# Performance work log

Measured on AMD Instinct MI355X. Metric: run time of the kernel, lower is better.

The kernel has to match this reference:

```python
import math
import jax, jax.numpy as jnp
import numpy as np
from jax import lax

B, S, D = 2, 1024, 768
H, E, DH = 12, 8, 64          # n_head, num_experts, head dim
KA = 1                        # top-k experts per head (attention)
KF = 2                        # top-k experts per token (FFN)
DFF = 2048
EMA_DECAY = 0.99
CAP_FACTOR = 1.25
NEG_INF = -1e9


def setup_inputs() -> dict:
    key = jax.random.key(0)
    ks = jax.random.split(key, 16)
    sc = 0.02
    x = jax.random.normal(ks[0], (B, S, D), jnp.float32)
    causal = jnp.tril(jnp.ones((S, S), jnp.float32))
    mask = jnp.where(causal > 0, 0.0, NEG_INF).astype(jnp.float32)
    return {
        "x": x,
        "mask": mask,
        "W_q": jax.random.normal(ks[1], (D, D), jnp.float32) * sc,
        "W_k": jax.random.normal(ks[2], (D, D), jnp.float32) * sc,
        "W_v": jax.random.normal(ks[3], (H, E, DH, DH), jnp.float32) * sc,
        "W_o": jax.random.normal(ks[4], (H, E, DH, DH), jnp.float32) * sc,
        "W_router": jax.random.normal(ks[5], (D, H * E), jnp.float32) * sc,
        "g1": jnp.ones((D,), jnp.float32),
        "b1": jnp.zeros((D,), jnp.float32),
        "g2": jnp.ones((D,), jnp.float32),
        "b2": jnp.zeros((D,), jnp.float32),
        "gate_ff": jax.random.normal(ks[6], (D, E), jnp.float32) * sc,
        "W1": jax.random.normal(ks[7], (E, D, DFF), jnp.float32) * sc,
        "W2": jax.random.normal(ks[8], (E, DFF, D), jnp.float32) * sc,
    }


def layer_norm(x, g, b, eps=1e-5):
    m = jnp.mean(x, -1, keepdims=True)
    v = jnp.var(x, -1, keepdims=True)
    return (x - m) * lax.rsqrt(v + eps) * g + b


def head_switch_attention(x, mask, W_q, W_k, W_v, W_o, W_router):
    b, s, d = x.shape
    q = (x @ W_q).reshape(b, s, H, DH)
    k = (x @ W_k).reshape(b, s, H, DH)
    scores = jnp.einsum("bshd,bthd->bhst", q, k) / math.sqrt(DH) + mask
    p_attn = jax.nn.softmax(scores, axis=-1)          # (B,H,S,S)
    gate_logits = (x @ W_router).reshape(b, s, H, E)
    topk_scores, topk_idx = lax.top_k(gate_logits, KA)  # (B,S,H,KA)
    probs = jax.nn.softmax(topk_scores, axis=-1)
    x_h = x.reshape(b, s, H, DH)
    # value projections for all experts (small d_h x d_h GEMMs)
    v_all = jnp.einsum("bshd,hedf->bshef", x_h, W_v)
    y = jnp.zeros_like(x_h)
    hard_counts = jnp.zeros((H, E), jnp.float32)
    for slot in range(KA):
        oh = jax.nn.one_hot(topk_idx[..., slot], E, dtype=x.dtype)  # (B,S,H,E)
        v_sel = jnp.einsum("bshef,bshe->bshf", v_all, oh)
        # faithful to original einsum 'bhst,hbsd->hbtd' (sums over s)
        attn_out = jnp.einsum("bhst,bshf->bthf", p_attn, v_sel)
        o_all = jnp.einsum("bthf,hefg->btheg", attn_out, W_o)
        o_sel = jnp.einsum("btheg,bthe->bthg", o_all, oh)
        y = y + o_sel * probs[..., slot][..., None]
        hard_counts = hard_counts + lax.stop_gradient(oh).sum((0, 1))
    y = y.reshape(b, s, d)
    # EMA buffers start at zero -> ema = (1-decay)*hard/denom
    ema = hard_counts / (b * s * KA) * (1.0 - EMA_DECAY)
    p_lb = ema / (ema.sum() + 1e-9)
    aux = (p_lb * p_lb).sum() * E * H
    return y, aux


def moe_ffn(x, gate_ff, W1, W2):
    b, s, d = x.shape
    gate_logits = x @ gate_ff                      # (B,S,E), eval: no noise
    topk_scores, topk_idx = lax.top_k(gate_logits, KF)
    probs = jax.nn.softmax(topk_scores, axis=-1)   # (B,S,KF)
    capacity = math.ceil(CAP_FACTOR * (b * s) / E)
    flat_idx = topk_idx.reshape(-1)                # (B*S*KF,)
    oh_flat = jax.nn.one_hot(flat_idx, E, dtype=jnp.float32)
    tokens_so_far = jnp.cumsum(oh_flat, axis=0)
    keep = jnp.take_along_axis(tokens_so_far <= capacity, flat_idx[:, None], axis=1)[:, 0]
    probs = probs * keep.reshape(b, s, KF).astype(probs.dtype)
    probs = probs / (probs.sum(-1, keepdims=True) + 1e-9)
    oh = jax.nn.one_hot(topk_idx, E, dtype=probs.dtype)   # (B,S,KF,E)
    w = (probs[..., None] * oh).sum(2).reshape(b * s, E)  # combined weight per (token, expert)
    xf = x.reshape(b * s, d)
    yf = jnp.zeros_like(xf)
    for e in range(E):
        # scaling applied BEFORE ReLU, matching original x_sel = x * weight
        xe = xf * w[:, e:e + 1]
        yf = yf + jnp.maximum(xe @ W1[e], 0.0) @ W2[e]
    token_ctr = ((probs > 0)[..., None].astype(jnp.float32) * oh).sum((0, 1, 2))
    imp_ctr = (probs[..., None] * oh).sum((0, 1, 2))
    aux = ((token_ctr / token_ctr.sum()) * (imp_ctr / imp_ctr.sum())).sum() * E
    return yf.reshape(b, s, d), aux


def reference(x, mask, W_q, W_k, W_v, W_o, W_router, g1, b1, g2, b2, gate_ff, W1, W2):
    # pre-norm transformer block: x + Attn(LN(x)); x + MoEFFN(LN(x))
    a, aux1 = head_switch_attention(layer_norm(x, g1, b1), mask, W_q, W_k, W_v, W_o, W_router)
    x1 = x + a  # dropout is identity in eval
    f, aux2 = moe_ffn(layer_norm(x1, g2, b2), gate_ff, W1, W2)
    return x1 + f, aux1 + aux2
```

## Files before the change

kernel.cpp:

```cpp
#include <hip/hip_runtime.h>
#include <hip/hip_bf16.h>
#include <cstdint>

typedef __hip_bfloat16 bf16;
typedef __attribute__((ext_vector_type(8))) __bf16 bfrag;
typedef __attribute__((ext_vector_type(4))) float f32x4;

#define B_    2
#define S_    1024
#define D_    768
#define H_    12
#define E_    8
#define DH_   64
#define DFF_  2048
#define CAP_  320
#define CAPP_ 384
#define NTOK  (B_*S_)
#define NTH   (NTOK*H_)
#define QKLD  1536
#define NHE   (H_*E_)

__device__ __forceinline__ void stage16(const bf16* g, bf16* ldsLane){
#if __has_builtin(__builtin_amdgcn_global_load_lds)
  __builtin_amdgcn_global_load_lds((const __attribute__((address_space(1))) unsigned int*)g,
                                   (__attribute__((address_space(3))) unsigned int*)ldsLane, 16, 0, 0);
#else
  *(bfrag*)ldsLane = *(const bfrag*)g;
#endif
}

__global__ __launch_bounds__(256)
void transp_qk(const float* __restrict__ Wq, const float* __restrict__ Wk, bf16* __restrict__ dst)
{
  const float* src = blockIdx.z ? Wk : Wq;
  int rowOff = blockIdx.z ? 768 : 0;
  __shared__ float t[32][33];
  int n0 = blockIdx.x*32, k0 = blockIdx.y*32;
  int tx = threadIdx.x & 31, ty = threadIdx.x >> 5;
#pragma unroll
  for (int r=0;r<4;r++)
    t[ty+r*8][tx] = src[(long)(k0 + ty + r*8)*D_ + n0 + tx];
  __syncthreads();
#pragma unroll
  for (int r=0;r<4;r++)
    dst[(long)(rowOff + n0 + ty + r*8)*D_ + k0 + tx] = __float2bfloat16(t[tx][ty+r*8]);
}

__global__ __launch_bounds__(256)
void transp_cvt(const float* __restrict__ src, bf16* __restrict__ dst,
                int K, int N, long sSrc, long sDst, int dstRowOff)
{
  src += (long)blockIdx.z*sSrc;
  dst += (long)blockIdx.z*sDst;
  __shared__ float t[32][33];
  int n0 = blockIdx.x*32, k0 = blockIdx.y*32;
  int tx = threadIdx.x & 31, ty = threadIdx.x >> 5;
#pragma unroll
  for (int r=0;r<4;r++){
    int kk = k0 + ty + r*8, nn = n0 + tx;
    t[ty+r*8][tx] = (nn < N) ? src[(long)kk*N + nn] : 0.f;
  }
  __syncthreads();
#pragma unroll
  for (int r=0;r<4;r++){
    int nn = n0 + ty + r*8;
    if (nn < N) dst[(long)(dstRowOff + nn)*K + k0 + tx] = __float2bfloat16(t[tx][ty+r*8]);
  }
}

__global__ __launch_bounds__(256)
void transp_f32(const float* __restrict__ src, float* __restrict__ dst, int K, int N)
{
  __shared__ float t[32][33];
  int n0 = blockIdx.x*32, k0 = blockIdx.y*32;
  int tx = threadIdx.x & 31, ty = threadIdx.x >> 5;
#pragma unroll
  for (int r=0;r<4;r++){
    int kk = k0 + ty + r*8, nn = n0 + tx;
    t[ty+r*8][tx] = (nn < N) ? src[(long)kk*N + nn] : 0.f;
  }
  __syncthreads();
#pragma unroll
  for (int r=0;r<4;r++){
    int nn = n0 + ty + r*8;
    if (nn < N) dst[(long)nn*K + k0 + tx] = t[tx][ty+r*8];
  }
}

__global__ __launch_bounds__(256)
void gemm_bn64(const bf16* __restrict__ A, const bf16* __restrict__ Bt,
               void* __restrict__ C, void* __restrict__ C2,
               int M, int N, int K, long sA, long sB, long sC, int relu, int outBf, int kSplit)
{
  int nwg = gridDim.x*gridDim.y*gridDim.z;
  int bid = blockIdx.x + gridDim.x*(blockIdx.y + gridDim.y*blockIdx.z);
  int nid = (bid & 7)*(nwg >> 3) + (bid >> 3);
  int bx = nid % gridDim.x;
  int t1 = nid / gridDim.x;
  int by = t1 % gridDim.y;
  int bz = t1 / gridDim.y;
  int e  = bz / kSplit, kc = bz - e*kSplit;
  A  += (long)e*sA;
  Bt += (long)e*sB;
  int kLen = K / kSplit, kBase = kc*kLen;
  int m0 = by*128, n0 = bx*64;
  __shared__ bf16 As[2][128*32];
  __shared__ bf16 Bs[2][64*32];
  int tid = threadIdx.x;
  int w = tid >> 6, lane = tid & 63;
  int quad = lane >> 4, l16 = lane & 15;
  int wm = w*32;
  f32x4 acc[2][4] = {};
  int srow = (lane >> 2);
  int gsw  = ((lane & 3) ^ (srow & 3))*8;
  const bf16* aBase = A + (long)m0*K;
  const bf16* bBase = Bt + (long)n0*K;
  int xr = (l16 & 3);
  int nIt = kLen >> 5;
  {
    int k0 = kBase;
#pragma unroll
    for (int j=0;j<2;j++){
      int c = w*2 + j, row = c*16 + srow;
      stage16(aBase + (long)row*K + k0 + gsw, As[0] + c*512 + lane*8);
    }
    int rowb = w*16 + srow;
    stage16(bBase + (long)rowb*K + k0 + gsw, Bs[0] + w*512 + lane*8);
  }
  int cur = 0;
  for (int it=0; it<nIt; ++it){
    __syncthreads();
    if (it+1 < nIt){
      int k0 = kBase + (it+1)*32;
      int nb = cur^1;
#pragma unroll
      for (int j=0;j<2;j++){
        int c = w*2 + j, row = c*16 + srow;
        stage16(aBase + (long)row*K + k0 + gsw, As[nb] + c*512 + lane*8);
      }
      int rowb = w*16 + srow;
      stage16(bBase + (long)rowb*K + k0 + gsw, Bs[nb] + w*512 + lane*8);
    }
    const bf16* Ac = As[cur];
    const bf16* Bc = Bs[cur];
    bfrag af[2], bfv[4];
#pragma unroll
    for (int t=0;t<2;t++) af[t]  = *(const bfrag*)(Ac + (wm + t*16 + l16)*32 + ((quad ^ xr)*8));
#pragma unroll
    for (int t=0;t<4;t++) bfv[t] = *(const bfrag*)(Bc + (t*16 + l16)*32 + ((quad ^ xr)*8));
#pragma unroll
    for (int ti=0;ti<2;ti++)
#pragma unroll
      for (int tj=0;tj<4;tj++)
        acc[ti][tj] = __builtin_amdgcn_mfma_f32_16x16x32_bf16(af[ti], bfv[tj], acc[ti][tj], 0, 0, 0);
    cur ^= 1;
  }
  long zoff = (long)e*sC;
  void* Cp = kc ? C2 : C;
  if (outBf){
    bf16* Cb = (bf16*)Cp + zoff;
#pragma unroll
    for (int ti=0;ti<2;ti++)
#pragma unroll
      for (int tj=0;tj<4;tj++)
#pragma unroll
        for (int r=0;r<4;r++){
          int row = m0 + wm + ti*16 + quad*4 + r;
          int col = n0 + tj*16 + l16;
          float v = acc[ti][tj][r];
          if (relu) v = fmaxf(v, 0.f);
          Cb[(long)row*N + col] = __float2bfloat16(v);
        }
  } else {
    float* Cf = (float*)Cp + zoff;
#pragma unroll
    for (int ti=0;ti<2;ti++)
#pragma unroll
      for (int tj=0;tj<4;tj++)
#pragma unroll
        for (int r=0;r<4;r++){
          int row = m0 + wm + ti*16 + quad*4 + r;
          int col = n0 + tj*16 + l16;
          float v = acc[ti][tj][r];
          if (relu) v = fmaxf(v, 0.f);
          Cf[(long)row*N + col] = v;
        }
  }
}

__global__ __launch_bounds__(256)
void ln_kernel(const float* __restrict__ src, const float* __restrict__ g, const float* __restrict__ bb,
               float* __restrict__ dstF, bf16* __restrict__ dstB,
               const float* __restrict__ gateW, float* __restrict__ glog2)
{
  int row = blockIdx.x, tid = threadIdx.x;
  __shared__ float red[256];
  __shared__ float gsum[4][E_];
  float v[3];
#pragma unroll
  for (int j=0;j<3;j++) v[j] = src[(long)row*D_ + tid + j*256];
  float s = v[0]+v[1]+v[2];
  red[tid]=s; __syncthreads();
  for (int o=128;o>0;o>>=1){ if(tid<o) red[tid]+=red[tid+o]; __syncthreads(); }
  float mean = red[0]*(1.0f/D_);
  __syncthreads();
  float sq = 0.f;
#pragma unroll
  for (int j=0;j<3;j++){ float d=v[j]-mean; sq += d*d; }
  red[tid]=sq; __syncthreads();
  for (int o=128;o>0;o>>=1){ if(tid<o) red[tid]+=red[tid+o]; __syncthreads(); }
  float rstd = rsqrtf(red[0]*(1.0f/D_) + 1e-5f);
  float ov[3];
#pragma unroll
  for (int j=0;j<3;j++){
    int d = tid + j*256;
    float o = (v[j]-mean)*rstd*g[d] + bb[d];
    ov[j] = o;
    dstF[(long)row*D_+d] = o;
    if (dstB) dstB[(long)row*D_+d] = __float2bfloat16(o);
  }
  if (gateW){
    float gp[E_] = {};
#pragma unroll
    for (int j=0;j<3;j++){
      int d = tid + j*256;
      const float* gw = gateW + (long)d*E_;
#pragma unroll
      for (int e=0;e<E_;e++) gp[e] += ov[j]*gw[e];
    }
#pragma unroll
    for (int off=1; off<64; off<<=1)
#pragma unroll
      for (int e=0;e<E_;e++) gp[e] += __shfl_xor(gp[e], off);
    if ((tid & 63) == 0)
#pragma unroll
      for (int e=0;e<E_;e++) gsum[tid>>6][e] = gp[e];
    __syncthreads();
    if (tid < E_)
      glog2[(long)row*E_ + tid] = gsum[0][tid]+gsum[1][tid]+gsum[2][tid]+gsum[3][tid];
  }
}

#define RTOK 4
__global__ __launch_bounds__(768)
void router_argmax(const float* __restrict__ ln1, const float* __restrict__ WrT,
                   int* __restrict__ eidx, int* __restrict__ gHist,
                   int* __restrict__ hCnt, int* __restrict__ hList)
{
  int tok0 = blockIdx.x*RTOK;
  int tid = threadIdx.x;
  int col = tid >> 3, seg = tid & 7;
  __shared__ float xrow[RTOK][D_];
  __shared__ float logits[RTOK][96];
  for (int i=tid; i<RTOK*D_; i+=768){
    int t = i / D_, dpos = i - t*D_;
    xrow[t][dpos] = ln1[(long)(tok0+t)*D_ + dpos];
  }
  __syncthreads();
  const float* wrow = WrT + (long)col*D_;
  float acc[RTOK] = {};
#pragma unroll
  for (int j=0;j<24;j++){
    int dbase = j*32 + seg*4;
    float4 w = *(const float4*)(wrow + dbase);
#pragma unroll
    for (int t=0;t<RTOK;t++){
      float4 xv = *(const float4*)(&xrow[t][dbase]);
      acc[t] += xv.x*w.x + xv.y*w.y + xv.z*w.z + xv.w*w.w;
    }
  }
#pragma unroll
  for (int off=1; off<8; off<<=1)
#pragma unroll
    for (int t=0;t<RTOK;t++) acc[t] += __shfl_xor(acc[t], off);
  if (seg == 0)
#pragma unroll
    for (int t=0;t<RTOK;t++) logits[t][col] = acc[t];
  __syncthreads();
  if (tid < RTOK*H_){
    int t = tid / H_, h = tid % H_;
    const float* p = &logits[t][h*8];
    float best = p[0]; int bi = 0;
#pragma unroll
    for (int e=1;e<8;e++){ float v=p[e]; if (v > best){ best=v; bi=e; } }
    int tok = tok0 + t;
    eidx[tok*H_ + h] = bi;
    atomicAdd(&gHist[h*E_ + bi], 1);
    int he = h*E_ + bi;
    int pos = atomicAdd(&hCnt[he], 1);
    hList[he*NTOK + pos] = tok;
  }
}

__global__ __launch_bounds__(256)
void vsel_b(const float* __restrict__ ln1, const float* __restrict__ Wv,
            const int* __restrict__ hCnt, const int* __restrict__ hList,
            bf16* __restrict__ vT)
{
  int he = blockIdx.x;
  int h = he >> 3;
  __shared__ float Ws[DH_*DH_];
  __shared__ float xsh[4][DH_];
  int tid = threadIdx.x;
  const float* W = Wv + (long)he*DH_*DH_;
  for (int i=tid; i<DH_*DH_; i+=256) Ws[i] = W[i];
  int cnt = hCnt[he];
  __syncthreads();
  int w = tid >> 6, lane = tid & 63;
  const int* lst = hList + (long)he*NTOK;
  for (int i = blockIdx.y*4 + w; i < cnt; i += 32){
    int tok = lst[i];
    int b = tok >> 10, s = tok & 1023;
    xsh[w][lane] = ln1[(long)tok*D_ + h*DH_ + lane];
    float acc = 0.f;
#pragma unroll 8
    for (int d=0; d<DH_; d++) acc += xsh[w][d]*Ws[d*DH_ + lane];
    vT[((long)(b*H_+h)*DH_ + lane)*S_ + s] = __float2bfloat16(acc);
  }
}

__global__ __launch_bounds__(256)
void attn_stats_mfma(const bf16* __restrict__ qkB, float* __restrict__ gM, float* __restrict__ gL)
{
  int s0 = blockIdx.x*64;
  int h = blockIdx.y, b = blockIdx.z;
  int tid = threadIdx.x;
  int w = tid >> 6, lane = tid & 63;
  int quad = lane >> 4, l16 = lane & 15;
  int x7 = l16 & 7;
  __shared__ bf16 ldsQ[64*64];
  __shared__ bf16 ldsK[2][64*64];
  const bf16* qbase = qkB + ((long)(b*S_ + s0))*QKLD + h*DH_;
  const bf16* kbase = qkB + ((long)(b*S_))*QKLD + 768 + h*DH_;
#pragma unroll
  for (int j=0;j<2;j++){
    int c = j*256 + tid;
    int row = c >> 3;
    int gs = ((c & 7) ^ (row & 7))*8;
    stage16(qbase + (long)row*QKLD + gs, ldsQ + c*8);
    stage16(kbase + (long)row*QKLD + gs, ldsK[0] + c*8);
  }
  float m_ln[4] = {-1e30f,-1e30f,-1e30f,-1e30f};
  float l_ln[4] = {0.f,0.f,0.f,0.f};
  int ttEnd = s0 >> 6;
  int cur = 0;
  for (int tt=0; tt<=ttEnd; tt++){
    __syncthreads();
    if (tt < ttEnd){
#pragma unroll
      for (int j=0;j<2;j++){
        int c = j*256 + tid;
        int row = c >> 3;
        int gs = ((c & 7) ^ (row & 7))*8;
        stage16(kbase + (long)((tt+1)*64 + row)*QKLD + gs, ldsK[cur^1] + c*8);
      }
    }
    const bf16* Kc = ldsK[cur];
    bfrag af0 = *(const bfrag*)(ldsQ + (w*16 + l16)*64 + ((quad     ^ x7)*8));
    bfrag af1 = *(const bfrag*)(ldsQ + (w*16 + l16)*64 + (((quad+4) ^ x7)*8));
    f32x4 cfr[4];
#pragma unroll
    for (int j=0;j<4;j++){
      bfrag b0 = *(const bfrag*)(Kc + (j*16 + l16)*64 + ((quad     ^ x7)*8));
      bfrag b1 = *(const bfrag*)(Kc + (j*16 + l16)*64 + (((quad+4) ^ x7)*8));
      f32x4 z = {};
      z = __builtin_amdgcn_mfma_f32_16x16x32_bf16(af0, b0, z, 0,0,0);
      z = __builtin_amdgcn_mfma_f32_16x16x32_bf16(af1, b1, z, 0,0,0);
      cfr[j] = z;
    }
#pragma unroll
    for (int r=0;r<4;r++){
      int s_g = s0 + w*16 + quad*4 + r;
      float v0 = (tt*64      + l16 <= s_g) ? cfr[0][r]*0.125f : -1e30f;
      float v1 = (tt*64 + 16 + l16 <= s_g) ? cfr[1][r]*0.125f : -1e30f;
      float v2 = (tt*64 + 32 + l16 <= s_g) ? cfr[2][r]*0.125f : -1e30f;
      float v3 = (tt*64 + 48 + l16 <= s_g) ? cfr[3][r]*0.125f : -1e30f;
      float mt = fmaxf(fmaxf(v0,v1), fmaxf(v2,v3));
      float mn = fmaxf(m_ln[r], mt);
      l_ln[r] = l_ln[r]*__expf(m_ln[r]-mn)
              + ((__expf(v0-mn)+__expf(v1-mn)) + (__expf(v2-mn)+__expf(v3-mn)));
      m_ln[r] = mn;
    }
    cur ^= 1;
  }
  float m_run[4], l_run[4];
#pragma unroll
  for (int r=0;r<4;r++){
    float mf = m_ln[r];
#pragma unroll
    for (int mm=1; mm<16; mm<<=1) mf = fmaxf(mf, __shfl_xor(mf, mm));
    float lf = l_ln[r]*__expf(m_ln[r]-mf);
#pragma unroll
    for (int mm=1; mm<16; mm<<=1) lf += __shfl_xor(lf, mm);
    m_run[r] = mf; l_run[r] = lf;
  }
  if (l16 == 0){
    long base = ((long)(b*H_ + h))*S_ + s0 + w*16 + quad*4;
#pragma unroll
    for (int r=0;r<4;r++){ gM[base+r] = m_run[r]; gL[base+r] = l_run[r]; }
  }
}

__global__ __launch_bounds__(256)
void attn_pv(const bf16* __restrict__ qkB, const bf16* __restrict__ vT,
             const float* __restrict__ gM, const float* __restrict__ gL, float* __restrict__ aoH)
{
  int t0 = blockIdx.x*64;
  int h = blockIdx.y, b = blockIdx.z;
  int bh = b*H_ + h;
  int tid = threadIdx.x;
  int w = tid >> 6, lane = tid & 63;
  int quad = lane >> 4, l16 = lane & 15;
  int x7 = l16 & 7;
  __shared__ bf16 ldsK[64*64];
  __shared__ bf16 ldsQ[2][64*64];
  __shared__ bf16 ldsV[2][64*64];
  __shared__ bf16 ldsS[64*72];
  __shared__ float smx[2][64], sli[2][64];
  const bf16* kbase = qkB + ((long)(b*S_ + t0))*QKLD + 768 + h*DH_;
  const bf16* qbase = qkB + ((long)(b*S_))*QKLD + h*DH_;
  const bf16* vbase = vT + ((long)bh*DH_)*S_;
  int sb0 = t0 >> 6;
#pragma unroll
  for (int j=0;j<2;j++){
    int c = j*256 + tid;
    int row = c >> 3;
    int gs = ((c & 7) ^ (row & 7))*8;
    stage16(kbase + (long)row*QKLD + gs, ldsK + c*8);
    stage16(qbase + (long)(sb0*64 + row)*QKLD + gs, ldsQ[0] + c*8);
    stage16(vbase + (long)row*S_ + sb0*64 + gs, ldsV[0] + c*8);
  }
  if (tid < 64){
    smx[0][tid] = gM[(long)bh*S_ + sb0*64 + tid];
    sli[0][tid] = 1.0f / gL[(long)bh*S_ + sb0*64 + tid];
  }
  f32x4 accO[4] = {};
  int cur = 0;
  for (int sb = sb0; sb < S_/64; sb++){
    __syncthreads();
    if (sb+1 < S_/64){
      int nb = cur^1;
#pragma unroll
      for (int j=0;j<2;j++){
        int c = j*256 + tid;
        int row = c >> 3;
        int gs = ((c & 7) ^ (row & 7))*8;
        stage16(qbase + (long)((sb+1)*64 + row)*QKLD + gs, ldsQ[nb] + c*8);
        stage16(vbase + (long)row*S_ + (sb+1)*64 + gs, ldsV[nb] + c*8);
      }
      if (tid < 64){
        smx[nb][tid] = gM[(long)bh*S_ + (sb+1)*64 + tid];
        sli[nb][tid] = 1.0f / gL[(long)bh*S_ + (sb+1)*64 + tid];
      }
    }
    const bf16* Qc = ldsQ[cur];
    const bf16* Vc = ldsV[cur];
    bfrag af0 = *(const bfrag*)(ldsK + (w*16 + l16)*64 + ((quad     ^ x7)*8));
    bfrag af1 = *(const bfrag*)(ldsK + (w*16 + l16)*64 + (((quad+4) ^ x7)*8));
    f32x4 cs[4];
#pragma unroll
    for (int j=0;j<4;j++){
      bfrag b0 = *(const bfrag*)(Qc + (j*16 + l16)*64 + ((quad     ^ x7)*8));
      bfrag b1 = *(const bfrag*)(Qc + (j*16 + l16)*64 + (((quad+4) ^ x7)*8));
      f32x4 z = {};
      z = __builtin_amdgcn_mfma_f32_16x16x32_bf16(af0, b0, z, 0,0,0);
      z = __builtin_amdgcn_mfma_f32_16x16x32_bf16(af1, b1, z, 0,0,0);
      cs[j] = z;
    }
#pragma unroll
    for (int j=0;j<4;j++)
#pragma unroll
      for (int r=0;r<4;r++){
        int t_loc = w*16 + quad*4 + r;
        int s_loc = j*16 + l16;
        float wgt = ((t0 + t_loc) <= (sb*64 + s_loc))
                  ? __expf(cs[j][r]*0.125f - smx[cur][s_loc])*sli[cur][s_loc] : 0.f;
        ldsS[t_loc*72 + s_loc] = __float2bfloat16(wgt);
      }
    bfrag pa0 = *(const bfrag*)(ldsS + (w*16 + l16)*72 + quad*8);
    bfrag pa1 = *(const bfrag*)(ldsS + (w*16 + l16)*72 + 32 + quad*8);
#pragma unroll
    for (int j=0;j<4;j++){
      bfrag b0 = *(const bfrag*)(Vc + (j*16 + l16)*64 + ((quad     ^ x7)*8));
      bfrag b1 = *(const bfrag*)(Vc + (j*16 + l16)*64 + (((quad+4) ^ x7)*8));
      accO[j] = __builtin_amdgcn_mfma_f32_16x16x32_bf16(pa0, b0, accO[j], 0,0,0);
      accO[j] = __builtin_amdgcn_mfma_f32_16x16x32_bf16(pa1, b1, accO[j], 0,0,0);
    }
    cur ^= 1;
  }
#pragma unroll
  for (int j=0;j<4;j++)
#pragma unroll
    for (int r=0;r<4;r++){
      int t_loc = w*16 + quad*4 + r;
      int f = j*16 + l16;
      aoH[((long)bh*S_ + t0 + t_loc)*DH_ + f] = accO[j][r];
    }
}

__global__ __launch_bounds__(256)
void oproj_b(const float* __restrict__ aoH, const float* __restrict__ Wo,
             const int* __restrict__ hCnt, const int* __restrict__ hList,
             const float* __restrict__ x, float* __restrict__ x1)
{
  int he = blockIdx.x;
  int h = he >> 3;
  __shared__ float Ws[DH_*DH_];
  __shared__ float xsh[4][DH_];
  int tid = threadIdx.x;
  const float* W = Wo + (long)he*DH_*DH_;
  for (int i=tid; i<DH_*DH_; i+=256) Ws[i] = W[i];
  int cnt = hCnt[he];
  __syncthreads();
  int w = tid >> 6, lane = tid & 63;
  const int* lst = hList + (long)he*NTOK;
  for (int i = blockIdx.y*4 + w; i < cnt; i += 32){
    int tok = lst[i];
    int b = tok >> 10, s = tok & 1023;
    xsh[w][lane] = aoH[((long)(b*H_+h)*S_ + s)*DH_ + lane];
    float acc = 0.f;
#pragma unroll 8
    for (int f=0; f<DH_; f++) acc += xsh[w][f]*Ws[f*DH_ + lane];
    long idx = (long)tok*D_ + h*DH_ + lane;
    x1[idx] = x[idx] + acc;
  }
}

__global__ __launch_bounds__(256)
void route_kernel(const float* __restrict__ glog2, const int* __restrict__ gHist,
                  int* __restrict__ gI0, int* __restrict__ gI1,
                  int* __restrict__ gPos0, int* __restrict__ gPos1,
                  int* __restrict__ listTok, float* __restrict__ listW,
                  int* __restrict__ gCnt, float* __restrict__ auxOut)
{
  __shared__ unsigned char sI0[NTOK], sI1[NTOK];
  __shared__ float sP0[NTOK], sP1[NTOK];
  __shared__ short sPos0[NTOK], sPos1[NTOK];
  __shared__ int   sScan[256*E_];
  __shared__ int   sHist[H_*E_];
  __shared__ float sImp[E_];
  __shared__ int   sCnt[E_];
  int tid = threadIdx.x;
  if (tid < E_) sImp[tid] = 0.f;
  if (tid < H_*E_) sHist[tid] = gHist[tid];
  for (int i=tid; i<NTOK; i+=256){
    const float* p = glog2 + (long)i*E_;
    float b0 = p[0]; int e0 = 0;
#pragma unroll
    for (int e=1;e<E_;e++){ float vv=p[e]; if (vv > b0){ b0=vv; e0=e; } }
    float b1v = -1e30f; int e1 = 0;
#pragma unroll
    for (int e=0;e<E_;e++){ if (e==e0) continue; float vv=p[e]; if (vv > b1v){ b1v=vv; e1=e; } }
    float ex = __expf(b1v - b0);
    float inv = 1.f/(1.f + ex);
    sI0[i] = (unsigned char)e0; sI1[i] = (unsigned char)e1;
    sP0[i] = inv; sP1[i] = ex*inv;
    gI0[i] = e0; gI1[i] = e1;
  }
  __syncthreads();
  {
    int myCnt[E_] = {};
#pragma unroll
    for (int j=0;j<16;j++){
      int i = tid*16 + j;
      int tok = i >> 1;
      int e = (i & 1) ? (int)sI1[tok] : (int)sI0[tok];
      myCnt[e]++;
    }
#pragma unroll
    for (int e=0;e<E_;e++) sScan[tid*E_+e] = myCnt[e];
    __syncthreads();
    for (int off=1; off<256; off<<=1){
      int v[E_];
      if (tid >= off){
#pragma unroll
        for (int e=0;e<E_;e++) v[e] = sScan[(tid-off)*E_+e];
      }
      __syncthreads();
      if (tid >= off){
#pragma unroll
        for (int e=0;e<E_;e++) sScan[tid*E_+e] += v[e];
      }
      __syncthreads();
    }
    int pref[E_];
#pragma unroll
    for (int e=0;e<E_;e++) pref[e] = tid ? sScan[(tid-1)*E_+e] : 0;
#pragma unroll
    for (int j=0;j<16;j++){
      int i = tid*16 + j;
      int tok = i >> 1;
      int e = (i & 1) ? (int)sI1[tok] : (int)sI0[tok];
      int pos = pref[e]++;
      short p = (pos < CAP_) ? (short)pos : (short)-1;
      if (i & 1) sPos1[tok] = p; else sPos0[tok] = p;
    }
    if (tid < E_){
      int cnt = sScan[255*E_ + tid];
      sCnt[tid] = cnt < CAP_ ? cnt : CAP_;
      gCnt[tid] = sCnt[tid];
    }
  }
  __syncthreads();
  for (int i=tid; i<NTOK; i+=256){
    int e0 = sI0[i], e1 = sI1[i];
    int p0i = sPos0[i], p1i = sPos1[i];
    float k0 = p0i >= 0 ? 1.f : 0.f, k1 = p1i >= 0 ? 1.f : 0.f;
    float p0 = sP0[i], p1 = sP1[i];
    float denom = p0*k0 + p1*k1 + 1e-9f;
    float w0 = p0*k0/denom, w1 = p1*k1/denom;
    if (p0i >= 0){ listTok[e0*CAP_+p0i] = i; listW[e0*CAP_+p0i] = w0; atomicAdd(&sImp[e0], w0); }
    if (p1i >= 0){ listTok[e1*CAP_+p1i] = i; listW[e1*CAP_+p1i] = w1; atomicAdd(&sImp[e1], w1); }
    gPos0[i] = p0i; gPos1[i] = p1i;
  }
  __syncthreads();
  if (tid == 0){
    float tot = 0.f;
    for (int i=0;i<H_*E_;i++) tot += (float)sHist[i]*(1.0f/NTOK)*0.01f;
    float a1 = 0.f;
    for (int i=0;i<H_*E_;i++){
      float p = ((float)sHist[i]*(1.0f/NTOK)*0.01f)/(tot + 1e-9f);
      a1 += p*p;
    }
    a1 *= (float)(H_*E_);
    float tcs = 0.f, ims = 0.f;
    for (int e=0;e<E_;e++){ tcs += (float)sCnt[e]; ims += sImp[e]; }
    float a2 = 0.f;
    for (int e=0;e<E_;e++) a2 += ((float)sCnt[e]/tcs)*(sImp[e]/ims);
    a2 *= (float)E_;
    auxOut[0] = a1 + a2;
  }
}

__global__ __launch_bounds__(256)
void gather_kernel(const float* __restrict__ ln2, const int* __restrict__ listTok,
                   const float* __restrict__ listW, const int* __restrict__ gCnt,
                   bf16* __restrict__ Xg)
{
  int blk = blockIdx.x;
  int e = blk / CAPP_, r = blk % CAPP_;
  int tid = threadIdx.x;
  bool live = r < gCnt[e];
  int tok = 0; float w = 0.f;
  if (live){ tok = listTok[e*CAP_+r]; w = listW[e*CAP_+r]; }
  for (int d=tid; d<D_; d+=256)
    Xg[(long)blk*D_ + d] = __float2bfloat16(live ? ln2[(long)tok*D_+d]*w : 0.f);
}

__global__ __launch_bounds__(256)
void combine_kernel(const float* __restrict__ x1,
                    const float* __restrict__ Ya, const float* __restrict__ Yb,
                    const int* __restrict__ gI0, const int* __restrict__ gI1,
                    const int* __restrict__ gPos0, const int* __restrict__ gPos1,
                    float* __restrict__ out)
{
  int i = blockIdx.x;
  int tid = threadIdx.x;
  int p0 = gPos0[i], p1 = gPos1[i];
  int e0 = gI0[i],  e1 = gI1[i];
  long off0 = (long)(e0*CAPP_ + (p0 >= 0 ? p0 : 0))*D_;
  long off1 = (long)(e1*CAPP_ + (p1 >= 0 ? p1 : 0))*D_;
  const float* y0a = Ya + off0; const float* y0b = Yb + off0;
  const float* y1a = Ya + off1; const float* y1b = Yb + off1;
  for (int d=tid; d<D_; d+=256){
    float v = x1[(long)i*D_+d];
    if (p0 >= 0) v += y0a[d] + y0b[d];
    if (p1 >= 0) v += y1a[d] + y1b[d];
    out[(long)i*D_+d] = v;
  }
}

extern "C" void kernel_launch(void* const* d_in, const int* in_sizes, int n_in,
                              void* d_out, int out_size, void* d_ws, size_t ws_size,
                              hipStream_t stream)
{
  const float* x    = (const float*)d_in[0];
  const float* W_q  = (const float*)d_in[2];
  const float* W_k  = (const float*)d_in[3];
  const float* W_v  = (const float*)d_in[4];
  const float* W_o  = (const float*)d_in[5];
  const float* W_r  = (const float*)d_in[6];
  const float* g1   = (const float*)d_in[7];
  const float* b1   = (const float*)d_in[8];
  const float* g2   = (const float*)d_in[9];
  const float* b2   = (const float*)d_in[10];
  const float* gate = (const float*)d_in[11];
  const float* W1   = (const float*)d_in[12];
  const float* W2   = (const float*)d_in[13];
  float* out = (float*)d_out;

  float* wsf = (float*)d_ws;
  const long oX1   = 0;
  const long oLnF  = 1572864;
  const long oLnB  = 3145728;
  const long oWcat = 3932160;
  const long oWrT  = 4521984;
  const long oHist = 4595712;
  const long oGM   = 4718592;
  const long oGL   = 4743168;
  const long oEidx = 4767744;
  const long oGlg2 = 4792320;
  const long oI0   = 4808704;
  const long oI1   = 4810752;
  const long oP0   = 4812800;
  const long oP1   = 4814848;
  const long oLT   = 4816896;
  const long oLW   = 4819456;
  const long oCnt  = 4822016;
  const long oHCnt = 4822100;
  const long SB    = 4822528;
  const long TOTAL = SB + 12976128;
  if (ws_size < (size_t)TOTAL*4) return;

  float* x1    = wsf + oX1;
  float* lnbF  = wsf + oLnF;
  bf16*  lnbB  = (bf16*)(wsf + oLnB);
  bf16*  WcatB = (bf16*)(wsf + oWcat);
  float* WrT   = wsf + oWrT;
  int*   gHist = (int*)(wsf + oHist);
  float* gM    = wsf + oGM;
  float* gL    = wsf + oGL;
  int*   eidx  = (int*)(wsf + oEidx);
  float* glog2 = wsf + oGlg2;
  int*   gI0   = (int*)(wsf + oI0);
  int*   gI1   = (int*)(wsf + oI1);
  int*   gPos0 = (int*)(wsf + oP0);
  int*   gPos1 = (int*)(wsf + oP1);
  int*   lTok  = (int*)(wsf + oLT);
  float* lW    = wsf + oLW;
  int*   gCnt  = (int*)(wsf + oCnt);
  int*   hCnt  = (int*)(wsf + oHCnt);
  bf16*  qkB   = (bf16*)(wsf + SB);
  bf16*  vT    = (bf16*)(wsf + SB + 1572864);
  float* aoH   = wsf + SB + 2359296;
  int*   hList = (int*)(wsf + SB + 3932160);
  bf16*  WT    = (bf16*)(wsf + SB);
  bf16*  Xg    = (bf16*)(wsf + SB + 6291456);
  bf16*  Hid   = (bf16*)(wsf + SB + 7471104);
  float* Yexp  = wsf + SB + 10616832;
  float* YexpB = wsf + oLnF;

  hipMemsetAsync(gHist, 0, H_*E_*sizeof(int), stream);
  hipMemsetAsync(hCnt, 0, NHE*sizeof(int), stream);
  transp_qk<<<dim3(24,24,2),256,0,stream>>>(W_q, W_k, WcatB);
  transp_f32<<<dim3(3,24,1),256,0,stream>>>(W_r, WrT, 768, 96);

  ln_kernel<<<NTOK,256,0,stream>>>(x, g1, b1, lnbF, lnbB, nullptr, nullptr);
  gemm_bn64<<<dim3(24,16,1),256,0,stream>>>(lnbB, WcatB, qkB, nullptr, 2048, QKLD, 768, 0,0,0, 0, 1, 1);
  router_argmax<<<NTOK/RTOK,768,0,stream>>>(lnbF, WrT, eidx, gHist, hCnt, hList);
  vsel_b<<<dim3(NHE,8,1),256,0,stream>>>(lnbF, W_v, hCnt, hList, vT);
  attn_stats_mfma<<<dim3(S_/64,H_,B_),256,0,stream>>>(qkB, gM, gL);
  attn_pv<<<dim3(S_/64,H_,B_),256,0,stream>>>(qkB, vT, gM, gL, aoH);
  oproj_b<<<dim3(NHE,8,1),256,0,stream>>>(aoH, W_o, hCnt, hList, x, x1);

  ln_kernel<<<NTOK,256,0,stream>>>(x1, g2, b2, lnbF, nullptr, gate, glog2);
  route_kernel<<<1,256,0,stream>>>(glog2, gHist, gI0,gI1,gPos0,gPos1, lTok,lW,gCnt, out + (size_t)NTOK*D_);
  gather_kernel<<<E_*CAPP_,256,0,stream>>>(lnbF, lTok, lW, gCnt, Xg);
  transp_cvt<<<dim3(64,24,8),256,0,stream>>>(W1, WT, 768, 2048, (long)768*2048, (long)2048*768, 0);
  gemm_bn64<<<dim3(32,3,8),256,0,stream>>>(Xg, WT, Hid, nullptr, CAPP_, DFF_, 768,
                                           (long)CAPP_*768, (long)2048*768, (long)CAPP_*2048, 1, 1, 1);
  transp_cvt<<<dim3(24,64,8),256,0,stream>>>(W2, WT, 2048, 768, (long)2048*768, (long)768*2048, 0);
  gemm_bn64<<<dim3(12,3,16),256,0,stream>>>(Hid, WT, Yexp, YexpB, CAPP_, 768, 2048,
                                            (long)CAPP_*2048, (long)768*2048, (long)CAPP_*768, 0, 0, 2);
  combine_kernel<<<NTOK,256,0,stream>>>(x1, Yexp, YexpB, gI0,gI1,gPos0,gPos1, out);
}
```

Baseline: 405.6 us.

## Merge weight transposes into one launch and pair causal attention tiles

```diff
diff --git a/kernel.cpp b/kernel.cpp
--- a/kernel.cpp
+++ b/kernel.cpp
@@ -30,60 +30,46 @@
 }
 
 __global__ __launch_bounds__(256)
-void transp_qk(const float* __restrict__ Wq, const float* __restrict__ Wk, bf16* __restrict__ dst)
-{
-  const float* src = blockIdx.z ? Wk : Wq;
-  int rowOff = blockIdx.z ? 768 : 0;
+void transp_all(const float* __restrict__ Wq, const float* __restrict__ Wk,
+                const float* __restrict__ Wr, const float* __restrict__ W1,
+                const float* __restrict__ W2,
+                bf16* __restrict__ WcatB, float* __restrict__ WrT,
+                bf16* __restrict__ WT1, bf16* __restrict__ WT2)
+{
   __shared__ float t[32][33];
-  int n0 = blockIdx.x*32, k0 = blockIdx.y*32;
+  int bid = blockIdx.x;
+  const float* src; int K, N, bx, by;
+  bf16* dstB = nullptr; float* dstF = nullptr;
+  if (bid < 1152){
+    int which = bid >= 576; int r = bid - which*576;
+    src = which ? Wk : Wq; K = 768; N = 768; bx = r % 24; by = r / 24;
+    dstB = WcatB + (long)(which ? 768 : 0)*768;
+  } else if (bid < 1224){
+    int r = bid - 1152; src = Wr; K = 768; N = 96; bx = r % 3; by = r / 3;
+    dstF = WrT;
+  } else if (bid < 13512){
+    int r = bid - 1224; int e = r / 1536; r -= e*1536;
+    src = W1 + (long)e*768*2048; K = 768; N = 2048; bx = r % 64; by = r / 64;
+    dstB = WT1 + (long)e*2048*768;
+  } else {
+    int r = bid - 13512; int e = r / 1536; r -= e*1536;
+    src = W2 + (long)e*2048*768; K = 2048; N = 768; bx = r % 24; by = r / 24;
+    dstB = WT2 + (long)e*768*2048;
+  }
+  int n0 = bx*32, k0 = by*32;
   int tx = threadIdx.x & 31, ty = threadIdx.x >> 5;
 #pragma unroll
   for (int r=0;r<4;r++)
-    t[ty+r*8][tx] = src[(long)(k0 + ty + r*8)*D_ + n0 + tx];
-  __syncthreads();
-#pragma unroll
-  for (int r=0;r<4;r++)
-    dst[(long)(rowOff + n0 + ty + r*8)*D_ + k0 + tx] = __float2bfloat16(t[tx][ty+r*8]);
-}
-
-__global__ __launch_bounds__(256)
-void transp_cvt(const float* __restrict__ src, bf16* __restrict__ dst,
-                int K, int N, long sSrc, long sDst, int dstRowOff)
-{
-  src += (long)blockIdx.z*sSrc;
-  dst += (long)blockIdx.z*sDst;
-  __shared__ float t[32][33];
-  int n0 = blockIdx.x*32, k0 = blockIdx.y*32;
-  int tx = threadIdx.x & 31, ty = threadIdx.x >> 5;
-#pragma unroll
-  for (int r=0;r<4;r++){
-    int kk = k0 + ty + r*8, nn = n0 + tx;
-    t[ty+r*8][tx] = (nn < N) ? src[(long)kk*N + nn] : 0.f;
-  }
-  __syncthreads();
-#pragma unroll
-  for (int r=0;r<4;r++){
-    int nn = n0 + ty + r*8;
-    if (nn < N) dst[(long)(dstRowOff + nn)*K + k0 + tx] = __float2bfloat16(t[tx][ty+r*8]);
-  }
-}
-
-__global__ __launch_bounds__(256)
-void transp_f32(const float* __restrict__ src, float* __restrict__ dst, int K, int N)
-{
-  __shared__ float t[32][33];
-  int n0 = blockIdx.x*32, k0 = blockIdx.y*32;
-  int tx = threadIdx.x & 31, ty = threadIdx.x >> 5;
-#pragma unroll
-  for (int r=0;r<4;r++){
-    int kk = k0 + ty + r*8, nn = n0 + tx;
-    t[ty+r*8][tx] = (nn < N) ? src[(long)kk*N + nn] : 0.f;
-  }
-  __syncthreads();
-#pragma unroll
-  for (int r=0;r<4;r++){
-    int nn = n0 + ty + r*8;
-    if (nn < N) dst[(long)nn*K + k0 + tx] = t[tx][ty+r*8];
+    t[ty+r*8][tx] = src[(long)(k0 + ty + r*8)*N + n0 + tx];
+  __syncthreads();
+  if (dstF){
+#pragma unroll
+    for (int r=0;r<4;r++)
+      dstF[(long)(n0 + ty + r*8)*K + k0 + tx] = t[tx][ty+r*8];
+  } else {
+#pragma unroll
+    for (int r=0;r<4;r++)
+      dstB[(long)(n0 + ty + r*8)*K + k0 + tx] = __float2bfloat16(t[tx][ty+r*8]);
   }
 }
 
@@ -322,7 +308,6 @@
 __global__ __launch_bounds__(256)
 void attn_stats_mfma(const bf16* __restrict__ qkB, float* __restrict__ gM, float* __restrict__ gL)
 {
-  int s0 = blockIdx.x*64;
   int h = blockIdx.y, b = blockIdx.z;
   int tid = threadIdx.x;
   int w = tid >> 6, lane = tid & 63;
@@ -330,74 +315,75 @@
   int x7 = l16 & 7;
   __shared__ bf16 ldsQ[64*64];
   __shared__ bf16 ldsK[2][64*64];
-  const bf16* qbase = qkB + ((long)(b*S_ + s0))*QKLD + h*DH_;
   const bf16* kbase = qkB + ((long)(b*S_))*QKLD + 768 + h*DH_;
-#pragma unroll
-  for (int j=0;j<2;j++){
-    int c = j*256 + tid;
-    int row = c >> 3;
-    int gs = ((c & 7) ^ (row & 7))*8;
-    stage16(qbase + (long)row*QKLD + gs, ldsQ + c*8);
-    stage16(kbase + (long)row*QKLD + gs, ldsK[0] + c*8);
-  }
-  float m_ln[4] = {-1e30f,-1e30f,-1e30f,-1e30f};
-  float l_ln[4] = {0.f,0.f,0.f,0.f};
-  int ttEnd = s0 >> 6;
-  int cur = 0;
-  for (int tt=0; tt<=ttEnd; tt++){
+  for (int half=0; half<2; half++){
+    int s0 = (half ? (S_/64 - 1 - blockIdx.x) : blockIdx.x)*64;
     __syncthreads();
-    if (tt < ttEnd){
-#pragma unroll
-      for (int j=0;j<2;j++){
-        int c = j*256 + tid;
-        int row = c >> 3;
-        int gs = ((c & 7) ^ (row & 7))*8;
-        stage16(kbase + (long)((tt+1)*64 + row)*QKLD + gs, ldsK[cur^1] + c*8);
-      }
-    }
-    const bf16* Kc = ldsK[cur];
-    bfrag af0 = *(const bfrag*)(ldsQ + (w*16 + l16)*64 + ((quad     ^ x7)*8));
-    bfrag af1 = *(const bfrag*)(ldsQ + (w*16 + l16)*64 + (((quad+4) ^ x7)*8));
-    f32x4 cfr[4];
-#pragma unroll
-    for (int j=0;j<4;j++){
-      bfrag b0 = *(const bfrag*)(Kc + (j*16 + l16)*64 + ((quad     ^ x7)*8));
-      bfrag b1 = *(const bfrag*)(Kc + (j*16 + l16)*64 + (((quad+4) ^ x7)*8));
-      f32x4 z = {};
-      z = __builtin_amdgcn_mfma_f32_16x16x32_bf16(af0, b0, z, 0,0,0);
-      z = __builtin_amdgcn_mfma_f32_16x16x32_bf16(af1, b1, z, 0,0,0);
-      cfr[j] = z;
+    const bf16* qbase = qkB + ((long)(b*S_ + s0))*QKLD + h*DH_;
+#pragma unroll
+    for (int j=0;j<2;j++){
+      int c = j*256 + tid;
+      int row = c >> 3;
+      int gs = ((c & 7) ^ (row & 7))*8;
+      stage16(qbase + (long)row*QKLD + gs, ldsQ + c*8);
+      stage16(kbase + (long)row*QKLD + gs, ldsK[0] + c*8);
+    }
+    float m_ln[4] = {-1e30f,-1e30f,-1e30f,-1e30f};
+    float l_ln[4] = {0.f,0.f,0.f,0.f};
+    int ttEnd = s0 >> 6;
+    int cur = 0;
+    for (int tt=0; tt<=ttEnd; tt++){
+      __syncthreads();
+      if (tt < ttEnd){
+#pragma unroll
+        for (int j=0;j<2;j++){
+          int c = j*256 + tid;
+          int row = c >> 3;
+          int gs = ((c & 7) ^ (row & 7))*8;
+          stage16(kbase + (long)((tt+1)*64 + row)*QKLD + gs, ldsK[cur^1] + c*8);
+        }
+      }
+      const bf16* Kc = ldsK[cur];
+      bfrag af0 = *(const bfrag*)(ldsQ + (w*16 + l16)*64 + ((quad     ^ x7)*8));
+      bfrag af1 = *(const bfrag*)(ldsQ + (w*16 + l16)*64 + (((quad+4) ^ x7)*8));
+      f32x4 cfr[4];
+#pragma unroll
+      for (int j=0;j<4;j++){
+        bfrag b0 = *(const bfrag*)(Kc + (j*16 + l16)*64 + ((quad     ^ x7)*8));
+        bfrag b1 = *(const bfrag*)(Kc + (j*16 + l16)*64 + (((quad+4) ^ x7)*8));
+        f32x4 z = {};
+        z = __builtin_amdgcn_mfma_f32_16x16x32_bf16(af0, b0, z, 0,0,0);
+        z = __builtin_amdgcn_mfma_f32_16x16x32_bf16(af1, b1, z, 0,0,0);
+        cfr[j] = z;
+      }
+#pragma unroll
+      for (int r=0;r<4;r++){
+        int s_g = s0 + w*16 + quad*4 + r;
+        float v0 = (tt*64      + l16 <= s_g) ? cfr[0][r]*0.125f : -1e30f;
+        float v1 = (tt*64 + 16 + l16 <= s_g) ? cfr[1][r]*0.125f : -1e30f;
+        float v2 = (tt*64 + 32 + l16 <= s_g) ? cfr[2][r]*0.125f : -1e30f;
+        float v3 = (tt*64 + 48 + l16 <= s_g) ? cfr[3][r]*0.125f : -1e30f;
+        float mt = fmaxf(fmaxf(v0,v1), fmaxf(v2,v3));
+        float mn = fmaxf(m_ln[r], mt);
+        l_ln[r] = l_ln[r]*__expf(m_ln[r]-mn)
+                + ((__expf(v0-mn)+__expf(v1-mn)) + (__expf(v2-mn)+__expf(v3-mn)));
+        m_ln[r] = mn;
+      }
+      cur ^= 1;
     }
 #pragma unroll
     for (int r=0;r<4;r++){
-      int s_g = s0 + w*16 + quad*4 + r;
-      float v0 = (tt*64      + l16 <= s_g) ? cfr[0][r]*0.125f : -1e30f;
-      float v1 = (tt*64 + 16 + l16 <= s_g) ? cfr[1][r]*0.125f : -1e30f;
-      float v2 = (tt*64 + 32 + l16 <= s_g) ? cfr[2][r]*0.125f : -1e30f;
-      float v3 = (tt*64 + 48 + l16 <= s_g) ? cfr[3][r]*0.125f : -1e30f;
-      float mt = fmaxf(fmaxf(v0,v1), fmaxf(v2,v3));
-      float mn = fmaxf(m_ln[r], mt);
-      l_ln[r] = l_ln[r]*__expf(m_ln[r]-mn)
-              + ((__expf(v0-mn)+__expf(v1-mn)) + (__expf(v2-mn)+__expf(v3-mn)));
-      m_ln[r] = mn;
-    }
-    cur ^= 1;
-  }
-  float m_run[4], l_run[4];
-#pragma unroll
-  for (int r=0;r<4;r++){
-    float mf = m_ln[r];
-#pragma unroll
-    for (int mm=1; mm<16; mm<<=1) mf = fmaxf(mf, __shfl_xor(mf, mm));
-    float lf = l_ln[r]*__expf(m_ln[r]-mf);
-#pragma unroll
-    for (int mm=1; mm<16; mm<<=1) lf += __shfl_xor(lf, mm);
-    m_run[r] = mf; l_run[r] = lf;
-  }
-  if (l16 == 0){
-    long base = ((long)(b*H_ + h))*S_ + s0 + w*16 + quad*4;
-#pragma unroll
-    for (int r=0;r<4;r++){ gM[base+r] = m_run[r]; gL[base+r] = l_run[r]; }
+      float mf = m_ln[r];
+#pragma unroll
+      for (int mm=1; mm<16; mm<<=1) mf = fmaxf(mf, __shfl_xor(mf, mm));
+      float lf = l_ln[r]*__expf(m_ln[r]-mf);
+#pragma unroll
+      for (int mm=1; mm<16; mm<<=1) lf += __shfl_xor(lf, mm);
+      if (l16 == 0){
+        long basei = ((long)(b*H_ + h))*S_ + s0 + w*16 + quad*4 + r;
+        gM[basei] = mf; gL[basei] = lf;
+      }
+    }
   }
 }
 
@@ -405,7 +391,6 @@
 void attn_pv(const bf16* __restrict__ qkB, const bf16* __restrict__ vT,
              const float* __restrict__ gM, const float* __restrict__ gL, float* __restrict__ aoH)
 {
-  int t0 = blockIdx.x*64;
   int h = blockIdx.y, b = blockIdx.z;
   int bh = b*H_ + h;
   int tid = threadIdx.x;
@@ -417,85 +402,89 @@
   __shared__ bf16 ldsV[2][64*64];
   __shared__ bf16 ldsS[64*72];
   __shared__ float smx[2][64], sli[2][64];
-  const bf16* kbase = qkB + ((long)(b*S_ + t0))*QKLD + 768 + h*DH_;
   const bf16* qbase = qkB + ((long)(b*S_))*QKLD + h*DH_;
   const bf16* vbase = vT + ((long)bh*DH_)*S_;
-  int sb0 = t0 >> 6;
-#pragma unroll
-  for (int j=0;j<2;j++){
-    int c = j*256 + tid;
-    int row = c >> 3;
-    int gs = ((c & 7) ^ (row & 7))*8;
-    stage16(kbase + (long)row*QKLD + gs, ldsK + c*8);
-    stage16(qbase + (long)(sb0*64 + row)*QKLD + gs, ldsQ[0] + c*8);
-    stage16(vbase + (long)row*S_ + sb0*64 + gs, ldsV[0] + c*8);
-  }
-  if (tid < 64){
-    smx[0][tid] = gM[(long)bh*S_ + sb0*64 + tid];
-    sli[0][tid] = 1.0f / gL[(long)bh*S_ + sb0*64 + tid];
-  }
-  f32x4 accO[4] = {};
-  int cur = 0;
-  for (int sb = sb0; sb < S_/64; sb++){
+  for (int half=0; half<2; half++){
+    int t0 = (half ? (S_/64 - 1 - blockIdx.x) : blockIdx.x)*64;
     __syncthreads();
-    if (sb+1 < S_/64){
-      int nb = cur^1;
-#pragma unroll
-      for (int j=0;j<2;j++){
-        int c = j*256 + tid;
-        int row = c >> 3;
-        int gs = ((c & 7) ^ (row & 7))*8;
-        stage16(qbase + (long)((sb+1)*64 + row)*QKLD + gs, ldsQ[nb] + c*8);
-        stage16(vbase + (long)row*S_ + (sb+1)*64 + gs, ldsV[nb] + c*8);
-      }
-      if (tid < 64){
-        smx[nb][tid] = gM[(long)bh*S_ + (sb+1)*64 + tid];
-        sli[nb][tid] = 1.0f / gL[(long)bh*S_ + (sb+1)*64 + tid];
-      }
-    }
-    const bf16* Qc = ldsQ[cur];
-    const bf16* Vc = ldsV[cur];
-    bfrag af0 = *(const bfrag*)(ldsK + (w*16 + l16)*64 + ((quad     ^ x7)*8));
-    bfrag af1 = *(const bfrag*)(ldsK + (w*16 + l16)*64 + (((quad+4) ^ x7)*8));
-    f32x4 cs[4];
-#pragma unroll
-    for (int j=0;j<4;j++){
-      bfrag b0 = *(const bfrag*)(Qc + (j*16 + l16)*64 + ((quad     ^ x7)*8));
-      bfrag b1 = *(const bfrag*)(Qc + (j*16 + l16)*64 + (((quad+4) ^ x7)*8));
-      f32x4 z = {};
-      z = __builtin_amdgcn_mfma_f32_16x16x32_bf16(af0, b0, z, 0,0,0);
-      z = __builtin_amdgcn_mfma_f32_16x16x32_bf16(af1, b1, z, 0,0,0);
-      cs[j] = z;
+    const bf16* kbase = qkB + ((long)(b*S_ + t0))*QKLD + 768 + h*DH_;
+    int sb0 = t0 >> 6;
+#pragma unroll
+    for (int j=0;j<2;j++){
+      int c = j*256 + tid;
+      int row = c >> 3;
+      int gs = ((c & 7) ^ (row & 7))*8;
+      stage16(kbase + (long)row*QKLD + gs, ldsK + c*8);
+      stage16(qbase + (long)(sb0*64 + row)*QKLD + gs, ldsQ[0] + c*8);
+      stage16(vbase + (long)row*S_ + sb0*64 + gs, ldsV[0] + c*8);
+    }
+    if (tid < 64){
+      smx[0][tid] = gM[(long)bh*S_ + sb0*64 + tid];
+      sli[0][tid] = 1.0f / gL[(long)bh*S_ + sb0*64 + tid];
+    }
+    f32x4 accO[4] = {};
+    int cur = 0;
+    for (int sb = sb0; sb < S_/64; sb++){
+      __syncthreads();
+      if (sb+1 < S_/64){
+        int nb = cur^1;
+#pragma unroll
+        for (int j=0;j<2;j++){
+          int c = j*256 + tid;
+          int row = c >> 3;
+          int gs = ((c & 7) ^ (row & 7))*8;
+          stage16(qbase + (long)((sb+1)*64 + row)*QKLD + gs, ldsQ[nb] + c*8);
+          stage16(vbase + (long)row*S_ + (sb+1)*64 + gs, ldsV[nb] + c*8);
+        }
+        if (tid < 64){
+          smx[nb][tid] = gM[(long)bh*S_ + (sb+1)*64 + tid];
+          sli[nb][tid] = 1.0f / gL[(long)bh*S_ + (sb+1)*64 + tid];
+        }
+      }
+      const bf16* Qc = ldsQ[cur];
+      const bf16* Vc = ldsV[cur];
+      bfrag af0 = *(const bfrag*)(ldsK + (w*16 + l16)*64 + ((quad     ^ x7)*8));
+      bfrag af1 = *(const bfrag*)(ldsK + (w*16 + l16)*64 + (((quad+4) ^ x7)*8));
+      f32x4 cs[4];
+#pragma unroll
+      for (int j=0;j<4;j++){
+        bfrag b0 = *(const bfrag*)(Qc + (j*16 + l16)*64 + ((quad     ^ x7)*8));
+        bfrag b1 = *(const bfrag*)(Qc + (j*16 + l16)*64 + (((quad+4) ^ x7)*8));
+        f32x4 z = {};
+        z = __builtin_amdgcn_mfma_f32_16x16x32_bf16(af0, b0, z, 0,0,0);
+        z = __builtin_amdgcn_mfma_f32_16x16x32_bf16(af1, b1, z, 0,0,0);
+        cs[j] = z;
+      }
+#pragma unroll
+      for (int j=0;j<4;j++)
+#pragma unroll
+        for (int r=0;r<4;r++){
+          int t_loc = w*16 + quad*4 + r;
+          int s_loc = j*16 + l16;
+          float wgt = ((t0 + t_loc) <= (sb*64 + s_loc))
+                    ? __expf(cs[j][r]*0.125f - smx[cur][s_loc])*sli[cur][s_loc] : 0.f;
+          ldsS[t_loc*72 + s_loc] = __float2bfloat16(wgt);
+        }
+      bfrag pa0 = *(const bfrag*)(ldsS + (w*16 + l16)*72 + quad*8);
+      bfrag pa1 = *(const bfrag*)(ldsS + (w*16 + l16)*72 + 32 + quad*8);
+#pragma unroll
+      for (int j=0;j<4;j++){
+        bfrag b0 = *(const bfrag*)(Vc + (j*16 + l16)*64 + ((quad     ^ x7)*8));
+        bfrag b1 = *(const bfrag*)(Vc + (j*16 + l16)*64 + (((quad+4) ^ x7)*8));
+        accO[j] = __builtin_amdgcn_mfma_f32_16x16x32_bf16(pa0, b0, accO[j], 0,0,0);
+        accO[j] = __builtin_amdgcn_mfma_f32_16x16x32_bf16(pa1, b1, accO[j], 0,0,0);
+      }
+      cur ^= 1;
     }
 #pragma unroll
     for (int j=0;j<4;j++)
 #pragma unroll
       for (int r=0;r<4;r++){
         int t_loc = w*16 + quad*4 + r;
-        int s_loc = j*16 + l16;
-        float wgt = ((t0 + t_loc) <= (sb*64 + s_loc))
-                  ? __expf(cs[j][r]*0.125f - smx[cur][s_loc])*sli[cur][s_loc] : 0.f;
-        ldsS[t_loc*72 + s_loc] = __float2bfloat16(wgt);
-      }
-    bfrag pa0 = *(const bfrag*)(ldsS + (w*16 + l16)*72 + quad*8);
-    bfrag pa1 = *(const bfrag*)(ldsS + (w*16 + l16)*72 + 32 + quad*8);
-#pragma unroll
-    for (int j=0;j<4;j++){
-      bfrag b0 = *(const bfrag*)(Vc + (j*16 + l16)*64 + ((quad     ^ x7)*8));
-      bfrag b1 = *(const bfrag*)(Vc + (j*16 + l16)*64 + (((quad+4) ^ x7)*8));
-      accO[j] = __builtin_amdgcn_mfma_f32_16x16x32_bf16(pa0, b0, accO[j], 0,0,0);
-      accO[j] = __builtin_amdgcn_mfma_f32_16x16x32_bf16(pa1, b1, accO[j], 0,0,0);
-    }
-    cur ^= 1;
-  }
-#pragma unroll
-  for (int j=0;j<4;j++)
-#pragma unroll
-    for (int r=0;r<4;r++){
-      int t_loc = w*16 + quad*4 + r;
-      int f = j*16 + l16;
-      aoH[((long)bh*S_ + t0 + t_loc)*DH_ + f] = accO[j][r];
-    }
+        int f = j*16 + l16;
+        aoH[((long)bh*S_ + t0 + t_loc)*DH_ + f] = accO[j][r];
+      }
+  }
 }
 
 __global__ __launch_bounds__(256)
@@ -696,6 +685,7 @@
   const long oWcat = 3932160;
   const long oWrT  = 4521984;
   const long oHist = 4595712;
+  const long oHCnt = 4595808;
   const long oGM   = 4718592;
   const long oGL   = 4743168;
   const long oEidx = 4767744;
@@ -707,9 +697,10 @@
   const long oLT   = 4816896;
   const long oLW   = 4819456;
   const long oCnt  = 4822016;
-  const long oHCnt = 4822100;
   const long SB    = 4822528;
-  const long TOTAL = SB + 12976128;
+  const long oWT1  = SB + 12976128;
+  const long oWT2  = oWT1 + 6291456;
+  const long TOTAL = oWT2 + 6291456;
   if (ws_size < (size_t)TOTAL*4) return;
 
   float* x1    = wsf + oX1;
@@ -718,6 +709,7 @@
   bf16*  WcatB = (bf16*)(wsf + oWcat);
   float* WrT   = wsf + oWrT;
   int*   gHist = (int*)(wsf + oHist);
+  int*   hCnt  = (int*)(wsf + oHCnt);
   float* gM    = wsf + oGM;
   float* gL    = wsf + oGL;
   int*   eidx  = (int*)(wsf + oEidx);
@@ -729,38 +721,34 @@
   int*   lTok  = (int*)(wsf + oLT);
   float* lW    = wsf + oLW;
   int*   gCnt  = (int*)(wsf + oCnt);
-  int*   hCnt  = (int*)(wsf + oHCnt);
   bf16*  qkB   = (bf16*)(wsf + SB);
   bf16*  vT    = (bf16*)(wsf + SB + 1572864);
   float* aoH   = wsf + SB + 2359296;
   int*   hList = (int*)(wsf + SB + 3932160);
-  bf16*  WT    = (bf16*)(wsf + SB);
   bf16*  Xg    = (bf16*)(wsf + SB + 6291456);
   bf16*  Hid   = (bf16*)(wsf + SB + 7471104);
   float* Yexp  = wsf + SB + 10616832;
   float* YexpB = wsf + oLnF;
-
-  hipMemsetAsync(gHist, 0, H_*E_*sizeof(int), stream);
-  hipMemsetAsync(hCnt, 0, NHE*sizeof(int), stream);
-  transp_qk<<<dim3(24,24,2),256,0,stream>>>(W_q, W_k, WcatB);
-  transp_f32<<<dim3(3,24,1),256,0,stream>>>(W_r, WrT, 768, 96);
+  bf16*  WT1   = (bf16*)(wsf + oWT1);
+  bf16*  WT2   = (bf16*)(wsf + oWT2);
+
+  hipMemsetAsync(gHist, 0, 2*NHE*sizeof(int), stream);
+  transp_all<<<25800,256,0,stream>>>(W_q, W_k, W_r, W1, W2, WcatB, WrT, WT1, WT2);
 
   ln_kernel<<<NTOK,256,0,stream>>>(x, g1, b1, lnbF, lnbB, nullptr, nullptr);
   gemm_bn64<<<dim3(24,16,1),256,0,stream>>>(lnbB, WcatB, qkB, nullptr, 2048, QKLD, 768, 0,0,0, 0, 1, 1);
   router_argmax<<<NTOK/RTOK,768,0,stream>>>(lnbF, WrT, eidx, gHist, hCnt, hList);
   vsel_b<<<dim3(NHE,8,1),256,0,stream>>>(lnbF, W_v, hCnt, hList, vT);
-  attn_stats_mfma<<<dim3(S_/64,H_,B_),256,0,stream>>>(qkB, gM, gL);
-  attn_pv<<<dim3(S_/64,H_,B_),256,0,stream>>>(qkB, vT, gM, gL, aoH);
+  attn_stats_mfma<<<dim3(S_/128,H_,B_),256,0,stream>>>(qkB, gM, gL);
+  attn_pv<<<dim3(S_/128,H_,B_),256,0,stream>>>(qkB, vT, gM, gL, aoH);
   oproj_b<<<dim3(NHE,8,1),256,0,stream>>>(aoH, W_o, hCnt, hList, x, x1);
 
   ln_kernel<<<NTOK,256,0,stream>>>(x1, g2, b2, lnbF, nullptr, gate, glog2);
   route_kernel<<<1,256,0,stream>>>(glog2, gHist, gI0,gI1,gPos0,gPos1, lTok,lW,gCnt, out + (size_t)NTOK*D_);
   gather_kernel<<<E_*CAPP_,256,0,stream>>>(lnbF, lTok, lW, gCnt, Xg);
-  transp_cvt<<<dim3(64,24,8),256,0,stream>>>(W1, WT, 768, 2048, (long)768*2048, (long)2048*768, 0);
-  gemm_bn64<<<dim3(32,3,8),256,0,stream>>>(Xg, WT, Hid, nullptr, CAPP_, DFF_, 768,
+  gemm_bn64<<<dim3(32,3,8),256,0,stream>>>(Xg, WT1, Hid, nullptr, CAPP_, DFF_, 768,
                                            (long)CAPP_*768, (long)2048*768, (long)CAPP_*2048, 1, 1, 1);
-  transp_cvt<<<dim3(24,64,8),256,0,stream>>>(W2, WT, 2048, 768, (long)2048*768, (long)768*2048, 0);
-  gemm_bn64<<<dim3(12,3,16),256,0,stream>>>(Hid, WT, Yexp, YexpB, CAPP_, 768, 2048,
+  gemm_bn64<<<dim3(12,3,16),256,0,stream>>>(Hid, WT2, Yexp, YexpB, CAPP_, 768, 2048,
                                             (long)CAPP_*2048, (long)768*2048, (long)CAPP_*768, 0, 0, 2);
   combine_kernel<<<NTOK,256,0,stream>>>(x1, Yexp, YexpB, gI0,gI1,gPos0,gPos1, out);
 }
```

Measured after the change: 398.1 us. Within noise of the previous version (-1.8%).
